# Kernel optimization log

Measured on AMD Instinct MI355X. Metric: run time of the kernel, lower is better.

The kernel has to match this reference:

```python
import jax, jax.numpy as jnp
import numpy as np

B, S, D = 4, 2048, 1024  # batch, seq_len, isize; FFN hidden = isize, gate dim = 2*isize


def setup_inputs() -> dict:
    key = jax.random.key(0)
    ks = jax.random.split(key, 6)
    sc = lambda n: 1.0 / np.sqrt(n)
    return {
        "iQ": jax.random.normal(ks[0], (B, S, D), jnp.float32),
        "iV": jax.random.normal(ks[1], (B, S, D), jnp.float32),
        "W1": jax.random.normal(ks[2], (D, D), jnp.float32) * sc(D),
        "b1": jnp.zeros((D,), jnp.float32),
        "W2": jax.random.normal(ks[3], (D, D), jnp.float32) * sc(D),
        "b2": jnp.zeros((D,), jnp.float32),
        "Wg": jax.random.normal(ks[4], (2 * D, 2 * D), jnp.float32) * sc(2 * D),
        "bg": jnp.zeros((2 * D,), jnp.float32),
    }


def reference(iQ, iV, W1, b1, W2, b2, Wg, bg):
    seql = iV.shape[1]
    # AAN cumulative-average matrix: row i has 1/(i+1) in cols 0..i (lower triangular)
    inv = 1.0 / jnp.arange(1, seql + 1, dtype=iV.dtype)  # [S]
    attn = jnp.tril(jnp.broadcast_to(inv[:, None], (seql, seql)))  # [S, S]
    avg = jnp.einsum('st,btd->bsd', attn, iV)  # [B, S, D]
    # PositionwiseFF with norm_input=False, dropout=0: Linear -> ReLU -> Linear
    h = jax.nn.relu(avg @ W1 + b1)
    ffn = h @ W2 + b2  # [B, S, D]
    # sigmoid gate over concat(iQ, ffn)
    g = jax.nn.sigmoid(jnp.concatenate([iQ, ffn], axis=-1) @ Wg + bg)  # [B, S, 2D]
    d = ffn.shape[-1]
    igate = g[..., :d]
    fgate = g[..., d:]
    return igate * iQ + fgate * ffn
```

## Files before the change

### kernel.cpp

```cpp
#include <hip/hip_runtime.h>
#include <hip/hip_bf16.h>
#include <cstdint>

typedef unsigned short u16;
typedef unsigned int   u32;

typedef __attribute__((ext_vector_type(8))) short short8;
typedef __attribute__((ext_vector_type(4))) float f32x4;

__device__ __forceinline__ float b2f(u16 v) { return __uint_as_float(((u32)v) << 16); }
__device__ __forceinline__ u16 f2b(float f) {
    u32 u = __float_as_uint(f);
    u += 0x7FFFu + ((u >> 16) & 1u);
    return (u16)(u >> 16);
}

#define G2L16(gp, lp) __builtin_amdgcn_global_load_lds(                       \
    (const __attribute__((address_space(1))) void*)(gp),                      \
    (__attribute__((address_space(3))) void*)(lp), 16, 0, 0)

__device__ __forceinline__ void transpose_body(const float* __restrict__ in,
                                               u16* __restrict__ out,
                                               int R, int C, int lb, int tilesX,
                                               float (*tile)[33]) {
    const int bx = (lb % tilesX) * 32;
    const int by = (lb / tilesX) * 32;
    const int tx = threadIdx.x & 31, ty = threadIdx.x >> 5;
    #pragma unroll
    for (int i = 0; i < 32; i += 8)
        tile[ty + i][tx] = in[(size_t)(by + ty + i) * C + (bx + tx)];
    __syncthreads();
    #pragma unroll
    for (int i = 0; i < 32; i += 8)
        out[(size_t)(bx + ty + i) * R + (by + tx)] = f2b(tile[tx][ty + i]);
}

__global__ void prologue_kernel(const float* __restrict__ W1, u16* __restrict__ W1t,
                                const float* __restrict__ W2, u16* __restrict__ W2t,
                                const float* __restrict__ Wg, u16* __restrict__ Wgt,
                                const float* __restrict__ iQ, u16* __restrict__ iQb,
                                const float* __restrict__ iV, float* __restrict__ csum) {
    __shared__ float tile[32][33];
    const int bid = blockIdx.x;
    const int tid = threadIdx.x;
    if (bid < 1024) {
        transpose_body(W1, W1t, 1024, 1024, bid, 32, tile);
    } else if (bid < 2048) {
        transpose_body(W2, W2t, 1024, 1024, bid - 1024, 32, tile);
    } else if (bid < 6144) {
        transpose_body(Wg, Wgt, 2048, 2048, bid - 2048, 64, tile);
    } else if (bid < 14336) {
        const size_t i = ((size_t)(bid - 6144) * 256 + tid) * 4;
        const float4 v = *(const float4*)(iQ + i);
        ushort4 o;
        o.x = f2b(v.x); o.y = f2b(v.y); o.z = f2b(v.z); o.w = f2b(v.w);
        *(ushort4*)(iQb + i) = o;
    } else {
        const int idx = bid - 14336;
        const int b = idx >> 7, c = idx & 127;
        const int d = tid * 4;
        const float* src = iV + ((size_t)(b * 2048 + c * 16)) * 1024 + d;
        float4 s = {0.f, 0.f, 0.f, 0.f};
        #pragma unroll 8
        for (int i = 0; i < 16; ++i) {
            const float4 v = *(const float4*)(src + (size_t)i * 1024);
            s.x += v.x; s.y += v.y; s.z += v.z; s.w += v.w;
        }
        *(float4*)(csum + ((size_t)(b * 128 + c)) * 1024 + d) = s;
    }
}

__global__ void scan_kernel(const float* __restrict__ iV, const float* __restrict__ csum,
                            u16* __restrict__ avg) {
    const int c = blockIdx.x & 127, b = blockIdx.x >> 7;
    const int d = threadIdx.x * 4;
    const float* cs = csum + (size_t)b * 128 * 1024 + d;
    float4 a0 = {0,0,0,0}, a1 = {0,0,0,0}, a2 = {0,0,0,0}, a3 = {0,0,0,0};
    int cc = 0;
    for (; cc + 4 <= c; cc += 4) {
        const float4 v0 = *(const float4*)(cs + (size_t)(cc + 0) * 1024);
        const float4 v1 = *(const float4*)(cs + (size_t)(cc + 1) * 1024);
        const float4 v2 = *(const float4*)(cs + (size_t)(cc + 2) * 1024);
        const float4 v3 = *(const float4*)(cs + (size_t)(cc + 3) * 1024);
        a0.x += v0.x; a0.y += v0.y; a0.z += v0.z; a0.w += v0.w;
        a1.x += v1.x; a1.y += v1.y; a1.z += v1.z; a1.w += v1.w;
        a2.x += v2.x; a2.y += v2.y; a2.z += v2.z; a2.w += v2.w;
        a3.x += v3.x; a3.y += v3.y; a3.z += v3.z; a3.w += v3.w;
    }
    for (; cc < c; ++cc) {
        const float4 v = *(const float4*)(cs + (size_t)cc * 1024);
        a0.x += v.x; a0.y += v.y; a0.z += v.z; a0.w += v.w;
    }
    float4 acc;
    acc.x = (a0.x + a1.x) + (a2.x + a3.x);
    acc.y = (a0.y + a1.y) + (a2.y + a3.y);
    acc.z = (a0.z + a1.z) + (a2.z + a3.z);
    acc.w = (a0.w + a1.w) + (a2.w + a3.w);

    const size_t off = ((size_t)(b * 2048 + c * 16)) * 1024 + d;
    const float* src = iV + off;
    u16*         dst = avg + off;
    const int s0 = c * 16;
    #pragma unroll 4
    for (int i = 0; i < 16; ++i) {
        const float4 v = *(const float4*)(src + (size_t)i * 1024);
        acc.x += v.x; acc.y += v.y; acc.z += v.z; acc.w += v.w;
        const float inv = 1.0f / (float)(s0 + i + 1);
        ushort4 o;
        o.x = f2b(acc.x * inv); o.y = f2b(acc.y * inv);
        o.z = f2b(acc.z * inv); o.w = f2b(acc.w * inv);
        *(ushort4*)(dst + (size_t)i * 1024) = o;
    }
}

template <int EPI>
__global__ __launch_bounds__(256, 2)
void gemm_kernel(const u16* __restrict__ A, const u16* __restrict__ Bt,
                 const float* __restrict__ bias, u16* __restrict__ C,
                 int M, int N, int K) {
    __shared__ u16 As[2][128 * 64];
    __shared__ u16 Bs[2][128 * 64];

    const int tid  = threadIdx.x;
    const int m0   = blockIdx.x * 128;
    const int n0   = blockIdx.y * 128;
    const int wave = tid >> 6, lane = tid & 63;
    const int wm   = (wave & 1) << 6;
    const int wn   = (wave >> 1) << 6;
    const int quad = lane >> 4, l16 = lane & 15;

    f32x4 acc[4][4];
    #pragma unroll
    for (int i = 0; i < 4; ++i)
        #pragma unroll
        for (int j = 0; j < 4; ++j) acc[i][j] = (f32x4){0.f, 0.f, 0.f, 0.f};

    int oo[4], rr[4], qq[4];
    #pragma unroll
    for (int j = 0; j < 4; ++j) {
        oo[j] = tid * 16 + j * 4096;
        rr[j] = oo[j] >> 7;
        qq[j] = ((oo[j] >> 4) & 7) ^ (rr[j] & 7);
    }

    const int ktiles = K >> 7;
    for (int kt = 0; kt < ktiles; ++kt) {
        const int kb = kt << 7;
        #pragma unroll
        for (int kk = 0; kk < 2; ++kk) {
            const int kbk = kb + kk * 64;
            #pragma unroll
            for (int j = 0; j < 4; ++j) {
                G2L16((const char*)A  + ((size_t)(m0 + rr[j]) * K + kbk) * 2 + qq[j] * 16,
                      (char*)&As[kk][0] + oo[j]);
                G2L16((const char*)Bt + ((size_t)(n0 + rr[j]) * K + kbk) * 2 + qq[j] * 16,
                      (char*)&Bs[kk][0] + oo[j]);
            }
        }
        __syncthreads();

        #pragma unroll
        for (int kk = 0; kk < 2; ++kk) {
            #pragma unroll
            for (int h = 0; h < 2; ++h) {
                short8 af[4], bf[4];
                #pragma unroll
                for (int mi = 0; mi < 4; ++mi) {
                    const int R = wm + mi * 16 + l16;
                    af[mi] = *(const short8*)(&As[kk][0] + R * 64 +
                                              ((((h << 2) | quad) ^ (R & 7)) << 3));
                }
                #pragma unroll
                for (int ni = 0; ni < 4; ++ni) {
                    const int R = wn + ni * 16 + l16;
                    bf[ni] = *(const short8*)(&Bs[kk][0] + R * 64 +
                                              ((((h << 2) | quad) ^ (R & 7)) << 3));
                }
                #pragma unroll
                for (int mi = 0; mi < 4; ++mi)
                    #pragma unroll
                    for (int ni = 0; ni < 4; ++ni)
                        acc[mi][ni] = __builtin_amdgcn_mfma_f32_16x16x32_bf16(
                            af[mi], bf[ni], acc[mi][ni], 0, 0, 0);
            }
        }
        __syncthreads();
    }

    #pragma unroll
    for (int ni = 0; ni < 4; ++ni) {
        const int col = n0 + wn + ni * 16 + l16;
        const float bv = bias[col];
        #pragma unroll
        for (int mi = 0; mi < 4; ++mi) {
            const int row0 = m0 + wm + mi * 16 + quad * 4;
            #pragma unroll
            for (int r = 0; r < 4; ++r) {
                float v = acc[mi][ni][r] + bv;
                if (EPI == 0) v = fmaxf(v, 0.f);
                C[(size_t)(row0 + r) * N + col] = f2b(v);
            }
        }
    }
}

__global__ __launch_bounds__(256, 2)
void gemm_gate_kernel(const u16* __restrict__ iQb, const u16* __restrict__ ffn,
                      const u16* __restrict__ Wgt, const float* __restrict__ bg,
                      const float* __restrict__ iQ, float* __restrict__ out,
                      int M, int D2 ) {
    __shared__ u16 As [128 * 64];
    __shared__ u16 Bs0[128 * 64];
    __shared__ u16 Bs1[128 * 64];

    const int tid  = threadIdx.x;
    const int m0   = blockIdx.x * 128;
    const int n0   = blockIdx.y * 128;
    const int wave = tid >> 6, lane = tid & 63;
    const int wm   = (wave & 1) << 6;
    const int wn   = (wave >> 1) << 6;
    const int quad = lane >> 4, l16 = lane & 15;
    const int D = D2 >> 1;

    f32x4 acc[2][4][4];
    #pragma unroll
    for (int p = 0; p < 2; ++p)
        #pragma unroll
        for (int i = 0; i < 4; ++i)
            #pragma unroll
            for (int j = 0; j < 4; ++j) acc[p][i][j] = (f32x4){0.f, 0.f, 0.f, 0.f};

    int oo[4], rr[4], qq[4];
    #pragma unroll
    for (int j = 0; j < 4; ++j) {
        oo[j] = tid * 16 + j * 4096;
        rr[j] = oo[j] >> 7;
        qq[j] = ((oo[j] >> 4) & 7) ^ (rr[j] & 7);
    }

    const int ktiles = D2 >> 6;
    for (int kt = 0; kt < ktiles; ++kt) {
        const int kb = kt << 6;
        const char* Ab = (const char*)((kb < D) ? (iQb + kb) : (ffn + (kb - D)));
        const char* B0 = (const char*)(Wgt + (size_t)n0 * D2 + kb);
        const char* B1 = (const char*)(Wgt + (size_t)(n0 + D) * D2 + kb);
        #pragma unroll
        for (int j = 0; j < 4; ++j) {
            G2L16(Ab + (size_t)(m0 + rr[j]) * D * 2 + qq[j] * 16, (char*)As  + oo[j]);
            G2L16(B0 + (size_t)rr[j] * D2 * 2 + qq[j] * 16,       (char*)Bs0 + oo[j]);
            G2L16(B1 + (size_t)rr[j] * D2 * 2 + qq[j] * 16,       (char*)Bs1 + oo[j]);
        }
        __syncthreads();

        #pragma unroll
        for (int h = 0; h < 2; ++h) {
            short8 af[4], bf0[4], bf1[4];
            #pragma unroll
            for (int mi = 0; mi < 4; ++mi) {
                const int R = wm + mi * 16 + l16;
                af[mi] = *(const short8*)(As + R * 64 + ((((h << 2) | quad) ^ (R & 7)) << 3));
            }
            #pragma unroll
            for (int ni = 0; ni < 4; ++ni) {
                const int R = wn + ni * 16 + l16;
                const int so = R * 64 + ((((h << 2) | quad) ^ (R & 7)) << 3);
                bf0[ni] = *(const short8*)(Bs0 + so);
                bf1[ni] = *(const short8*)(Bs1 + so);
            }
            #pragma unroll
            for (int mi = 0; mi < 4; ++mi)
                #pragma unroll
                for (int ni = 0; ni < 4; ++ni) {
                    acc[0][mi][ni] = __builtin_amdgcn_mfma_f32_16x16x32_bf16(
                        af[mi], bf0[ni], acc[0][mi][ni], 0, 0, 0);
                    acc[1][mi][ni] = __builtin_amdgcn_mfma_f32_16x16x32_bf16(
                        af[mi], bf1[ni], acc[1][mi][ni], 0, 0, 0);
                }
        }
        __syncthreads();
    }

    #pragma unroll
    for (int ni = 0; ni < 4; ++ni) {
        const int col = n0 + wn + ni * 16 + l16;
        const float bgi = bg[col];
        const float bgf = bg[col + D];
        #pragma unroll
        for (int mi = 0; mi < 4; ++mi) {
            const int row0 = m0 + wm + mi * 16 + quad * 4;
            #pragma unroll
            for (int r = 0; r < 4; ++r) {
                const size_t idx = (size_t)(row0 + r) * D + col;
                const float gi = 1.0f / (1.0f + __expf(-(acc[0][mi][ni][r] + bgi)));
                const float gf = 1.0f / (1.0f + __expf(-(acc[1][mi][ni][r] + bgf)));
                out[idx] = gi * iQ[idx] + gf * b2f(ffn[idx]);
            }
        }
    }
}

extern "C" void kernel_launch(void* const* d_in, const int* in_sizes, int n_in,
                              void* d_out, int out_size, void* d_ws, size_t ws_size,
                              hipStream_t stream) {
    const int B = 4, S = 2048, D = 1024, D2 = 2048;
    const int M = B * S;

    const float* iQ = (const float*)d_in[0];
    const float* iV = (const float*)d_in[1];
    const float* W1 = (const float*)d_in[2];
    const float* b1 = (const float*)d_in[3];
    const float* W2 = (const float*)d_in[4];
    const float* b2 = (const float*)d_in[5];
    const float* Wg = (const float*)d_in[6];
    const float* bg = (const float*)d_in[7];
    float* out = (float*)d_out;

    u16*   regA = (u16*)d_ws;
    u16*   regB = regA + (size_t)M * D;
    u16*   iQb  = regB + (size_t)M * D;
    u16*   W1t  = iQb  + (size_t)M * D;
    u16*   W2t  = W1t  + (size_t)D * D;
    u16*   Wgt  = W2t  + (size_t)D * D;
    float* csum = (float*)(Wgt + (size_t)D2 * D2);

    u16* avg = regA;
    u16* ffn = regA;
    u16* h   = regB;

    prologue_kernel<<<14848, 256, 0, stream>>>(W1, W1t, W2, W2t, Wg, Wgt,
                                               iQ, iQb, iV, csum);
    scan_kernel<<<B * 128, 256, 0, stream>>>(iV, csum, avg);
    gemm_kernel<0><<<dim3(M / 128, D / 128), 256, 0, stream>>>(avg, W1t, b1, h, M, D, D);
    gemm_kernel<1><<<dim3(M / 128, D / 128), 256, 0, stream>>>(h, W2t, b2, ffn, M, D, D);
    gemm_gate_kernel<<<dim3(M / 128, D / 128), 256, 0, stream>>>(
        iQb, ffn, Wgt, bg, iQ, out, M, D2);
}
```

Before: 262.1 us.

## Fuse all stages into one persistent kernel with software grid barriers

Replaces five separate launches (prologue, scan, two FFN GEMMs, gate GEMM) with a single persistent kernel of 512 blocks that runs each stage in turn and separates them with an atomic-counter grid barrier. Each block takes a fixed slice of every stage, for example 12 transpose tiles and one 128x128 GEMM tile. This removes launch gaps and per-kernel tails between stages. In exchange it relies on all 512 blocks being co-resident (2 per CU at 64KB LDS each). Static per-block assignment can also load-balance worse than the hardware scheduler did across the many prologue blocks, and it adds a memset launch.

```diff
diff --git a/kernel.cpp b/kernel.cpp
--- a/kernel.cpp
+++ b/kernel.cpp
@@ -18,6 +18,27 @@
 #define G2L16(gp, lp) __builtin_amdgcn_global_load_lds(                       \
     (const __attribute__((address_space(1))) void*)(gp),                      \
     (__attribute__((address_space(3))) void*)(lp), 16, 0, 0)
+
+__device__ __forceinline__ void grid_barrier(u32* bar, u32* gen, u32 nb) {
+    __syncthreads();
+    if (threadIdx.x == 0) {
+        __threadfence();
+        const u32 g = __hip_atomic_load(gen, __ATOMIC_RELAXED,
+                                        __HIP_MEMORY_SCOPE_AGENT);
+        const u32 t = atomicAdd(bar, 1u);
+        if (t == nb - 1u) {
+            *bar = 0u;
+            __threadfence();
+            atomicAdd(gen, 1u);
+        } else {
+            while (__hip_atomic_load(gen, __ATOMIC_RELAXED,
+                                     __HIP_MEMORY_SCOPE_AGENT) == g)
+                __builtin_amdgcn_s_sleep(4);
+        }
+        __threadfence();
+    }
+    __syncthreads();
+}
 
 __device__ __forceinline__ void transpose_body(const float* __restrict__ in,
                                                u16* __restrict__ out,
@@ -35,95 +56,15 @@
         out[(size_t)(bx + ty + i) * R + (by + tx)] = f2b(tile[tx][ty + i]);
 }
 
-__global__ void prologue_kernel(const float* __restrict__ W1, u16* __restrict__ W1t,
-                                const float* __restrict__ W2, u16* __restrict__ W2t,
-                                const float* __restrict__ Wg, u16* __restrict__ Wgt,
-                                const float* __restrict__ iQ, u16* __restrict__ iQb,
-                                const float* __restrict__ iV, float* __restrict__ csum) {
-    __shared__ float tile[32][33];
-    const int bid = blockIdx.x;
-    const int tid = threadIdx.x;
-    if (bid < 1024) {
-        transpose_body(W1, W1t, 1024, 1024, bid, 32, tile);
-    } else if (bid < 2048) {
-        transpose_body(W2, W2t, 1024, 1024, bid - 1024, 32, tile);
-    } else if (bid < 6144) {
-        transpose_body(Wg, Wgt, 2048, 2048, bid - 2048, 64, tile);
-    } else if (bid < 14336) {
-        const size_t i = ((size_t)(bid - 6144) * 256 + tid) * 4;
-        const float4 v = *(const float4*)(iQ + i);
-        ushort4 o;
-        o.x = f2b(v.x); o.y = f2b(v.y); o.z = f2b(v.z); o.w = f2b(v.w);
-        *(ushort4*)(iQb + i) = o;
-    } else {
-        const int idx = bid - 14336;
-        const int b = idx >> 7, c = idx & 127;
-        const int d = tid * 4;
-        const float* src = iV + ((size_t)(b * 2048 + c * 16)) * 1024 + d;
-        float4 s = {0.f, 0.f, 0.f, 0.f};
-        #pragma unroll 8
-        for (int i = 0; i < 16; ++i) {
-            const float4 v = *(const float4*)(src + (size_t)i * 1024);
-            s.x += v.x; s.y += v.y; s.z += v.z; s.w += v.w;
-        }
-        *(float4*)(csum + ((size_t)(b * 128 + c)) * 1024 + d) = s;
-    }
-}
-
-__global__ void scan_kernel(const float* __restrict__ iV, const float* __restrict__ csum,
-                            u16* __restrict__ avg) {
-    const int c = blockIdx.x & 127, b = blockIdx.x >> 7;
-    const int d = threadIdx.x * 4;
-    const float* cs = csum + (size_t)b * 128 * 1024 + d;
-    float4 a0 = {0,0,0,0}, a1 = {0,0,0,0}, a2 = {0,0,0,0}, a3 = {0,0,0,0};
-    int cc = 0;
-    for (; cc + 4 <= c; cc += 4) {
-        const float4 v0 = *(const float4*)(cs + (size_t)(cc + 0) * 1024);
-        const float4 v1 = *(const float4*)(cs + (size_t)(cc + 1) * 1024);
-        const float4 v2 = *(const float4*)(cs + (size_t)(cc + 2) * 1024);
-        const float4 v3 = *(const float4*)(cs + (size_t)(cc + 3) * 1024);
-        a0.x += v0.x; a0.y += v0.y; a0.z += v0.z; a0.w += v0.w;
-        a1.x += v1.x; a1.y += v1.y; a1.z += v1.z; a1.w += v1.w;
-        a2.x += v2.x; a2.y += v2.y; a2.z += v2.z; a2.w += v2.w;
-        a3.x += v3.x; a3.y += v3.y; a3.z += v3.z; a3.w += v3.w;
-    }
-    for (; cc < c; ++cc) {
-        const float4 v = *(const float4*)(cs + (size_t)cc * 1024);
-        a0.x += v.x; a0.y += v.y; a0.z += v.z; a0.w += v.w;
-    }
-    float4 acc;
-    acc.x = (a0.x + a1.x) + (a2.x + a3.x);
-    acc.y = (a0.y + a1.y) + (a2.y + a3.y);
-    acc.z = (a0.z + a1.z) + (a2.z + a3.z);
-    acc.w = (a0.w + a1.w) + (a2.w + a3.w);
-
-    const size_t off = ((size_t)(b * 2048 + c * 16)) * 1024 + d;
-    const float* src = iV + off;
-    u16*         dst = avg + off;
-    const int s0 = c * 16;
-    #pragma unroll 4
-    for (int i = 0; i < 16; ++i) {
-        const float4 v = *(const float4*)(src + (size_t)i * 1024);
-        acc.x += v.x; acc.y += v.y; acc.z += v.z; acc.w += v.w;
-        const float inv = 1.0f / (float)(s0 + i + 1);
-        ushort4 o;
-        o.x = f2b(acc.x * inv); o.y = f2b(acc.y * inv);
-        o.z = f2b(acc.z * inv); o.w = f2b(acc.w * inv);
-        *(ushort4*)(dst + (size_t)i * 1024) = o;
-    }
-}
-
 template <int EPI>
-__global__ __launch_bounds__(256, 2)
-void gemm_kernel(const u16* __restrict__ A, const u16* __restrict__ Bt,
-                 const float* __restrict__ bias, u16* __restrict__ C,
-                 int M, int N, int K) {
-    __shared__ u16 As[2][128 * 64];
-    __shared__ u16 Bs[2][128 * 64];
-
-    const int tid  = threadIdx.x;
-    const int m0   = blockIdx.x * 128;
-    const int n0   = blockIdx.y * 128;
+__device__ __forceinline__ void gemm128_phase(const u16* __restrict__ A,
+                                              const u16* __restrict__ Bt,
+                                              const float* __restrict__ bias,
+                                              u16* __restrict__ C,
+                                              u16 (*lds)[8192], int b, int tid) {
+    const int K = 1024, N = 1024;
+    const int m0   = (b & 63) * 128;
+    const int n0   = (b >> 6) * 128;
     const int wave = tid >> 6, lane = tid & 63;
     const int wm   = (wave & 1) << 6;
     const int wn   = (wave >> 1) << 6;
@@ -143,8 +84,7 @@
         qq[j] = ((oo[j] >> 4) & 7) ^ (rr[j] & 7);
     }
 
-    const int ktiles = K >> 7;
-    for (int kt = 0; kt < ktiles; ++kt) {
+    for (int kt = 0; kt < (K >> 7); ++kt) {
         const int kb = kt << 7;
         #pragma unroll
         for (int kk = 0; kk < 2; ++kk) {
@@ -152,9 +92,9 @@
             #pragma unroll
             for (int j = 0; j < 4; ++j) {
                 G2L16((const char*)A  + ((size_t)(m0 + rr[j]) * K + kbk) * 2 + qq[j] * 16,
-                      (char*)&As[kk][0] + oo[j]);
+                      (char*)&lds[kk][0] + oo[j]);
                 G2L16((const char*)Bt + ((size_t)(n0 + rr[j]) * K + kbk) * 2 + qq[j] * 16,
-                      (char*)&Bs[kk][0] + oo[j]);
+                      (char*)&lds[2 + kk][0] + oo[j]);
             }
         }
         __syncthreads();
@@ -167,13 +107,13 @@
                 #pragma unroll
                 for (int mi = 0; mi < 4; ++mi) {
                     const int R = wm + mi * 16 + l16;
-                    af[mi] = *(const short8*)(&As[kk][0] + R * 64 +
+                    af[mi] = *(const short8*)(&lds[kk][0] + R * 64 +
                                               ((((h << 2) | quad) ^ (R & 7)) << 3));
                 }
                 #pragma unroll
                 for (int ni = 0; ni < 4; ++ni) {
                     const int R = wn + ni * 16 + l16;
-                    bf[ni] = *(const short8*)(&Bs[kk][0] + R * 64 +
+                    bf[ni] = *(const short8*)(&lds[2 + kk][0] + R * 64 +
                                               ((((h << 2) | quad) ^ (R & 7)) << 3));
                 }
                 #pragma unroll
@@ -204,23 +144,20 @@
     }
 }
 
-__global__ __launch_bounds__(256, 2)
-void gemm_gate_kernel(const u16* __restrict__ iQb, const u16* __restrict__ ffn,
-                      const u16* __restrict__ Wgt, const float* __restrict__ bg,
-                      const float* __restrict__ iQ, float* __restrict__ out,
-                      int M, int D2 ) {
-    __shared__ u16 As [128 * 64];
-    __shared__ u16 Bs0[128 * 64];
-    __shared__ u16 Bs1[128 * 64];
-
-    const int tid  = threadIdx.x;
-    const int m0   = blockIdx.x * 128;
-    const int n0   = blockIdx.y * 128;
+__device__ __forceinline__ void gate_phase(const u16* __restrict__ iQb,
+                                           const u16* __restrict__ ffn,
+                                           const u16* __restrict__ Wgt,
+                                           const float* __restrict__ bg,
+                                           const float* __restrict__ iQ,
+                                           float* __restrict__ out,
+                                           u16 (*lds)[8192], int b, int tid) {
+    const int D2 = 2048, D = 1024;
+    const int m0   = (b & 63) * 128;
+    const int n0   = (b >> 6) * 128;
     const int wave = tid >> 6, lane = tid & 63;
     const int wm   = (wave & 1) << 6;
     const int wn   = (wave >> 1) << 6;
     const int quad = lane >> 4, l16 = lane & 15;
-    const int D = D2 >> 1;
 
     f32x4 acc[2][4][4];
     #pragma unroll
@@ -238,17 +175,16 @@
         qq[j] = ((oo[j] >> 4) & 7) ^ (rr[j] & 7);
     }
 
-    const int ktiles = D2 >> 6;
-    for (int kt = 0; kt < ktiles; ++kt) {
+    for (int kt = 0; kt < (D2 >> 6); ++kt) {
         const int kb = kt << 6;
         const char* Ab = (const char*)((kb < D) ? (iQb + kb) : (ffn + (kb - D)));
         const char* B0 = (const char*)(Wgt + (size_t)n0 * D2 + kb);
         const char* B1 = (const char*)(Wgt + (size_t)(n0 + D) * D2 + kb);
         #pragma unroll
         for (int j = 0; j < 4; ++j) {
-            G2L16(Ab + (size_t)(m0 + rr[j]) * D * 2 + qq[j] * 16, (char*)As  + oo[j]);
-            G2L16(B0 + (size_t)rr[j] * D2 * 2 + qq[j] * 16,       (char*)Bs0 + oo[j]);
-            G2L16(B1 + (size_t)rr[j] * D2 * 2 + qq[j] * 16,       (char*)Bs1 + oo[j]);
+            G2L16(Ab + (size_t)(m0 + rr[j]) * D * 2 + qq[j] * 16, (char*)&lds[0][0] + oo[j]);
+            G2L16(B0 + (size_t)rr[j] * D2 * 2 + qq[j] * 16,       (char*)&lds[1][0] + oo[j]);
+            G2L16(B1 + (size_t)rr[j] * D2 * 2 + qq[j] * 16,       (char*)&lds[2][0] + oo[j]);
         }
         __syncthreads();
 
@@ -258,14 +194,15 @@
             #pragma unroll
             for (int mi = 0; mi < 4; ++mi) {
                 const int R = wm + mi * 16 + l16;
-                af[mi] = *(const short8*)(As + R * 64 + ((((h << 2) | quad) ^ (R & 7)) << 3));
+                af[mi] = *(const short8*)(&lds[0][0] + R * 64 +
+                                          ((((h << 2) | quad) ^ (R & 7)) << 3));
             }
             #pragma unroll
             for (int ni = 0; ni < 4; ++ni) {
                 const int R = wn + ni * 16 + l16;
                 const int so = R * 64 + ((((h << 2) | quad) ^ (R & 7)) << 3);
-                bf0[ni] = *(const short8*)(Bs0 + so);
-                bf1[ni] = *(const short8*)(Bs1 + so);
+                bf0[ni] = *(const short8*)(&lds[1][0] + so);
+                bf1[ni] = *(const short8*)(&lds[2][0] + so);
             }
             #pragma unroll
             for (int mi = 0; mi < 4; ++mi)
@@ -299,19 +236,120 @@
     }
 }
 
+__global__ __launch_bounds__(256, 2)
+void mega_kernel(const float* __restrict__ W1, const float* __restrict__ W2,
+                 const float* __restrict__ Wg, const float* __restrict__ iQ,
+                 const float* __restrict__ iV, const float* __restrict__ b1,
+                 const float* __restrict__ b2, const float* __restrict__ bg,
+                 float* __restrict__ out, u16* __restrict__ W1t,
+                 u16* __restrict__ W2t, u16* __restrict__ Wgt,
+                 u16* __restrict__ iQb, float* __restrict__ csum,
+                 u16* __restrict__ regA, u16* __restrict__ regB,
+                 u32* __restrict__ bar) {
+    __shared__ u16 lds[4][8192];
+
+    const int b   = blockIdx.x;
+    const int tid = threadIdx.x;
+    u32* gen = bar + 1;
+
+    {
+        float (*tile)[33] = (float (*)[33])(&lds[0][0]);
+        #pragma unroll 1
+        for (int t = 0; t < 12; ++t) {
+            const int task = b * 12 + t;
+            if (task < 1024)      transpose_body(W1, W1t, 1024, 1024, task, 32, tile);
+            else if (task < 2048) transpose_body(W2, W2t, 1024, 1024, task - 1024, 32, tile);
+            else                  transpose_body(Wg, Wgt, 2048, 2048, task - 2048, 64, tile);
+            __syncthreads();
+        }
+        #pragma unroll 1
+        for (int t = 0; t < 16; ++t) {
+            const size_t i = ((size_t)(b * 16 + t) * 256 + tid) * 4;
+            const float4 v = *(const float4*)(iQ + i);
+            ushort4 o;
+            o.x = f2b(v.x); o.y = f2b(v.y); o.z = f2b(v.z); o.w = f2b(v.w);
+            *(ushort4*)(iQb + i) = o;
+        }
+        {
+            const int bb = b >> 7, c = b & 127;
+            const int d = tid * 4;
+            const float* src = iV + ((size_t)(bb * 2048 + c * 16)) * 1024 + d;
+            float4 s = {0.f, 0.f, 0.f, 0.f};
+            #pragma unroll 8
+            for (int i2 = 0; i2 < 16; ++i2) {
+                const float4 v = *(const float4*)(src + (size_t)i2 * 1024);
+                s.x += v.x; s.y += v.y; s.z += v.z; s.w += v.w;
+            }
+            *(float4*)(csum + ((size_t)(bb * 128 + c)) * 1024 + d) = s;
+        }
+    }
+    grid_barrier(bar, gen, 512);
+
+    {
+        const int c = b & 127, bb = b >> 7;
+        const int d = tid * 4;
+        const float* cs = csum + (size_t)bb * 128 * 1024 + d;
+        float4 a0 = {0,0,0,0}, a1 = {0,0,0,0}, a2 = {0,0,0,0}, a3 = {0,0,0,0};
+        int cc = 0;
+        for (; cc + 4 <= c; cc += 4) {
+            const float4 v0 = *(const float4*)(cs + (size_t)(cc + 0) * 1024);
+            const float4 v1 = *(const float4*)(cs + (size_t)(cc + 1) * 1024);
+            const float4 v2 = *(const float4*)(cs + (size_t)(cc + 2) * 1024);
+            const float4 v3 = *(const float4*)(cs + (size_t)(cc + 3) * 1024);
+            a0.x += v0.x; a0.y += v0.y; a0.z += v0.z; a0.w += v0.w;
+            a1.x += v1.x; a1.y += v1.y; a1.z += v1.z; a1.w += v1.w;
+            a2.x += v2.x; a2.y += v2.y; a2.z += v2.z; a2.w += v2.w;
+            a3.x += v3.x; a3.y += v3.y; a3.z += v3.z; a3.w += v3.w;
+        }
+        for (; cc < c; ++cc) {
+            const float4 v = *(const float4*)(cs + (size_t)cc * 1024);
+            a0.x += v.x; a0.y += v.y; a0.z += v.z; a0.w += v.w;
+        }
+        float4 acc;
+        acc.x = (a0.x + a1.x) + (a2.x + a3.x);
+        acc.y = (a0.y + a1.y) + (a2.y + a3.y);
+        acc.z = (a0.z + a1.z) + (a2.z + a3.z);
+        acc.w = (a0.w + a1.w) + (a2.w + a3.w);
+
+        const size_t off = ((size_t)(bb * 2048 + c * 16)) * 1024 + d;
+        const float* src = iV + off;
+        u16*         dst = regA + off;
+        const int s0 = c * 16;
+        #pragma unroll 4
+        for (int i2 = 0; i2 < 16; ++i2) {
+            const float4 v = *(const float4*)(src + (size_t)i2 * 1024);
+            acc.x += v.x; acc.y += v.y; acc.z += v.z; acc.w += v.w;
+            const float inv = 1.0f / (float)(s0 + i2 + 1);
+            ushort4 o;
+            o.x = f2b(acc.x * inv); o.y = f2b(acc.y * inv);
+            o.z = f2b(acc.z * inv); o.w = f2b(acc.w * inv);
+            *(ushort4*)(dst + (size_t)i2 * 1024) = o;
+        }
+    }
+    grid_barrier(bar, gen, 512);
+
+    gemm128_phase<0>(regA, W1t, b1, regB, lds, b, tid);
+    grid_barrier(bar, gen, 512);
+
+    gemm128_phase<1>(regB, W2t, b2, regA, lds, b, tid);
+    grid_barrier(bar, gen, 512);
+
+    gate_phase(iQb, regA, Wgt, bg, iQ, out, lds, b, tid);
+}
+
 extern "C" void kernel_launch(void* const* d_in, const int* in_sizes, int n_in,
                               void* d_out, int out_size, void* d_ws, size_t ws_size,
                               hipStream_t stream) {
-    const int B = 4, S = 2048, D = 1024, D2 = 2048;
-    const int M = B * S;
-
+    const int D = 1024, D2 = 2048;
+    const int M = 8192;
+
+    const float* W1 = (const float*)d_in[2];
+    const float* W2 = (const float*)d_in[4];
+    const float* Wg = (const float*)d_in[6];
     const float* iQ = (const float*)d_in[0];
     const float* iV = (const float*)d_in[1];
-    const float* W1 = (const float*)d_in[2];
     const float* b1 = (const float*)d_in[3];
-    const float* W2 = (const float*)d_in[4];
     const float* b2 = (const float*)d_in[5];
-    const float* Wg = (const float*)d_in[6];
     const float* bg = (const float*)d_in[7];
     float* out = (float*)d_out;
 
@@ -322,16 +360,10 @@
     u16*   W2t  = W1t  + (size_t)D * D;
     u16*   Wgt  = W2t  + (size_t)D * D;
     float* csum = (float*)(Wgt + (size_t)D2 * D2);
-
-    u16* avg = regA;
-    u16* ffn = regA;
-    u16* h   = regB;
-
-    prologue_kernel<<<14848, 256, 0, stream>>>(W1, W1t, W2, W2t, Wg, Wgt,
-                                               iQ, iQb, iV, csum);
-    scan_kernel<<<B * 128, 256, 0, stream>>>(iV, csum, avg);
-    gemm_kernel<0><<<dim3(M / 128, D / 128), 256, 0, stream>>>(avg, W1t, b1, h, M, D, D);
-    gemm_kernel<1><<<dim3(M / 128, D / 128), 256, 0, stream>>>(h, W2t, b2, ffn, M, D, D);
-    gemm_gate_kernel<<<dim3(M / 128, D / 128), 256, 0, stream>>>(
-        iQb, ffn, Wgt, bg, iQ, out, M, D2);
-}
+    u32*   bar  = (u32*)(csum + (size_t)4 * 128 * 1024);
+
+    hipMemsetAsync(bar, 0, 2 * sizeof(u32), stream);
+    mega_kernel<<<512, 256, 0, stream>>>(W1, W2, Wg, iQ, iV, b1, b2, bg, out,
+                                         W1t, W2t, Wgt, iQb, csum,
+                                         regA, regB, bar);
+}
```

New measurement: 519.0 us. 98.0% more time.
